# Performance work log

Hardware: AMD Instinct MI355X
Metric: run time of the kernel (lower is better)

The kernel has to match this reference:

```python
import jax, jax.numpy as jnp
import numpy as np

D_MODEL = 1024
B, S = 4, 4096


def setup_inputs() -> dict:
    key = jax.random.key(0)
    k1, k2, k3, k4, k5 = jax.random.split(key, 5)
    lim = 1.0 / np.sqrt(D_MODEL)  # nn.Linear default init range
    x = jax.random.normal(k1, (B, S, D_MODEL), dtype=jnp.float32)
    mask = jnp.ones((B, S), dtype=jnp.float32)
    W_up = jax.random.uniform(k2, (D_MODEL, D_MODEL), jnp.float32, -lim, lim)
    b_up = jax.random.uniform(k3, (D_MODEL,), jnp.float32, -lim, lim)
    W_f = jax.random.uniform(k4, (D_MODEL, D_MODEL), jnp.float32, -lim, lim)
    b_f = jax.random.uniform(k5, (D_MODEL,), jnp.float32, -lim, lim)
    decay_param = jnp.zeros((1,), dtype=jnp.float32)
    return {"x": x, "mask": mask, "W_up": W_up, "b_up": b_up,
            "W_f": W_f, "b_f": b_f, "decay_param": decay_param}


def _decay_scan(u, decay):
    # h_t = decay * h_{t-1} + u_t  along axis=1, via associative scan.
    # Element: (a, b) representing h -> a*h + b; compose: (a1*a2, b1*a2 + b2).
    a = jnp.broadcast_to(decay, u.shape)

    def combine(c1, c2):
        a1, b1 = c1
        a2, b2 = c2
        return a1 * a2, b1 * a2 + b2

    _, h = jax.lax.associative_scan(combine, (a, u), axis=1)
    return h


def reference(x, mask, W_up, b_up, W_f, b_f, decay_param):
    decay = jax.nn.sigmoid(decay_param)[0]
    # u_i = mask_i * linear_update(x_i)
    u = (jnp.einsum('bsd,ed->bse', x, W_up) + b_up) * mask[..., None]
    # h_t = sum_{i<=t} decay^(t-i) * u_i  (exponential-decay recurrence)
    h = _decay_scan(u, decay)
    return jnp.einsum('bsd,ed->bse', h, W_f) + b_f
```

## Files before the change

### kernel.cpp

```cpp
#include <hip/hip_runtime.h>
#include <hip/hip_bf16.h>
#include <cstdint>
#include <cstddef>

#define DMODEL 1024
#define BATCH  4
#define SEQ    4096
#define BSROWS (BATCH*SEQ)
#define CHUNK  32
#define NCHUNK (SEQ/CHUNK)
#define NCH_T  (BATCH*NCHUNK)

typedef __attribute__((ext_vector_type(8))) short bf16x8;
typedef __attribute__((ext_vector_type(4))) float f32x4;


__device__ __forceinline__ unsigned short f2bf(float f) {
  union { float f; uint32_t u; } v; v.f = f;
  uint32_t u = v.u;
  u += 0x7FFFu + ((u >> 16) & 1u);
  return (unsigned short)(u >> 16);
}

__device__ __forceinline__ float sigmoid_dev(const float* dp) {
  return 1.0f / (1.0f + expf(-dp[0]));
}

typedef __attribute__((address_space(1))) void void_g;
typedef __attribute__((address_space(3))) void void_l;

__device__ __forceinline__ void gl2lds16(const void* g, void* l) {
  __builtin_amdgcn_global_load_lds((void_g*)g, (void_l*)l, 16, 0, 0);
}

__device__ __forceinline__ void kloop64(
    const unsigned short* __restrict__ A, const unsigned short* __restrict__ B,
    int m0, int n0, f32x4 acc[2][2],
    unsigned short* As, unsigned short* Bs, int tid) {
  int lane = tid & 63, w = tid >> 6, wm = w & 1, wn = w >> 1;
  int quad = lane >> 4, l16 = lane & 15;
  int r = tid >> 3, cch = tid & 7;
  int g = cch ^ (r & 7);

  auto stage = [&](int t, int slot) {
    int k0 = t * 64;
    unsigned short* dA = As + slot * 4096;
    unsigned short* dB = Bs + slot * 4096;
    gl2lds16(A + (size_t)(m0 + r) * DMODEL + k0 + g * 8,      dA + r * 64 + cch * 8);
    gl2lds16(A + (size_t)(m0 + 32 + r) * DMODEL + k0 + g * 8, dA + (32 + r) * 64 + cch * 8);
    gl2lds16(B + (size_t)(n0 + r) * DMODEL + k0 + g * 8,      dB + r * 64 + cch * 8);
    gl2lds16(B + (size_t)(n0 + 32 + r) * DMODEL + k0 + g * 8, dB + (32 + r) * 64 + cch * 8);
  };
  auto compute = [&](int slot) {
    const bf16x8* Av = (const bf16x8*)(As + slot * 4096);
    const bf16x8* Bv = (const bf16x8*)(Bs + slot * 4096);
    #pragma unroll
    for (int kk = 0; kk < 2; ++kk) {
      bf16x8 af[2], bfr[2];
      #pragma unroll
      for (int i = 0; i < 2; ++i) {
        int rowA = wm * 32 + i * 16 + l16;
        af[i]  = Av[rowA * 8 + ((kk * 4 + quad) ^ (l16 & 7))];
        int rowB = wn * 32 + i * 16 + l16;
        bfr[i] = Bv[rowB * 8 + ((kk * 4 + quad) ^ (l16 & 7))];
      }
      __builtin_amdgcn_s_setprio(1);
      #pragma unroll
      for (int i = 0; i < 2; ++i)
        #pragma unroll
        for (int j = 0; j < 2; ++j)
          acc[i][j] = __builtin_amdgcn_mfma_f32_16x16x32_bf16(af[i], bfr[j], acc[i][j], 0, 0, 0);
      __builtin_amdgcn_s_setprio(0);
    }
  };

  stage(0, 0); stage(1, 1);
  asm volatile("s_waitcnt vmcnt(4)" ::: "memory");
  __builtin_amdgcn_s_barrier();
  asm volatile("" ::: "memory");
  int cur = 0;
  for (int t = 0; t < 14; ++t) {
    int ns = cur + 2; if (ns >= 3) ns -= 3;
    stage(t + 2, ns);
    compute(cur);
    asm volatile("s_waitcnt vmcnt(4)" ::: "memory");
    __builtin_amdgcn_s_barrier();
    asm volatile("" ::: "memory");
    cur = (cur == 2) ? 0 : cur + 1;
  }
  compute(cur);
  asm volatile("s_waitcnt vmcnt(0)" ::: "memory");
  __builtin_amdgcn_s_barrier();
  asm volatile("" ::: "memory");
  cur = (cur == 2) ? 0 : cur + 1;
  compute(cur);
}

__global__ __launch_bounds__(256) void prep_kernel(
    const float* __restrict__ x, const float* __restrict__ mask,
    const float* __restrict__ W_up, const float* __restrict__ b_up,
    const float* __restrict__ W_f, const float* __restrict__ dp,
    unsigned short* __restrict__ Wf_bf, unsigned short* __restrict__ WupT,
    float* __restrict__ bb, unsigned short* __restrict__ hv,
    float* __restrict__ carry, float* __restrict__ lbeta,
    float* __restrict__ cbeta) {
  __shared__ float tile[32][33];
  int blk = blockIdx.x;
  int tid = threadIdx.x;

  if (blk < 512) {
    float decay = sigmoid_dev(dp);
    int b = blk / NCHUNK, c = blk % NCHUNK;
    int base = b * SEQ + c * CHUNK;
    const float4* xp = (const float4*)(x + (size_t)base * DMODEL);
    const float4* mp4 = (const float4*)(mask + base);
    float mreg[32];
    #pragma unroll
    for (int q = 0; q < 8; ++q) {
      float4 t = mp4[q];
      mreg[q * 4 + 0] = t.x; mreg[q * 4 + 1] = t.y;
      mreg[q * 4 + 2] = t.z; mreg[q * 4 + 3] = t.w;
    }
    float4 h = make_float4(0.f, 0.f, 0.f, 0.f);
    #pragma unroll
    for (int s = 0; s < CHUNK; ++s) {
      float m = mreg[s];
      float4 xv = xp[(size_t)s * (DMODEL / 4) + tid];
      h.x = decay * h.x + m * xv.x;
      h.y = decay * h.y + m * xv.y;
      h.z = decay * h.z + m * xv.z;
      h.w = decay * h.w + m * xv.w;
      ushort4 o;
      o.x = f2bf(h.x); o.y = f2bf(h.y); o.z = f2bf(h.z); o.w = f2bf(h.w);
      ((ushort4*)hv)[(size_t)(base + s) * (DMODEL / 4) + tid] = o;
    }
    ((float4*)carry)[(size_t)blk * (DMODEL / 4) + tid] = h;
  } else if (blk < 1536) {
    int e = blk - 512;
    int lane = tid & 63, w = tid >> 6;
    float4 v = ((const float4*)(W_f + (size_t)e * DMODEL))[tid];
    float4 bu = ((const float4*)b_up)[tid];
    ushort4 o;
    o.x = f2bf(v.x); o.y = f2bf(v.y); o.z = f2bf(v.z); o.w = f2bf(v.w);
    ((ushort4*)(Wf_bf + (size_t)e * DMODEL))[tid] = o;
    float s = v.x * bu.x + v.y * bu.y + v.z * bu.z + v.w * bu.w;
    #pragma unroll
    for (int off = 32; off; off >>= 1) s += __shfl_down(s, off);
    if (lane == 0) ((float*)tile)[w] = s;
    __syncthreads();
    if (tid == 0)
      bb[e] = ((float*)tile)[0] + ((float*)tile)[1] +
              ((float*)tile)[2] + ((float*)tile)[3];
  } else if (blk < 2560) {
    int id = blk - 1536;
    int bx = id & 31, by = id >> 5;
    int tx = tid & 31, ty = tid >> 5;
    int xx = bx * 32 + tx;
    int y0 = by * 32;
    for (int j = ty; j < 32; j += 8)
      tile[j][tx] = W_up[(size_t)(y0 + j) * DMODEL + xx];
    __syncthreads();
    int dd = tid >> 3;
    int c4 = (tid & 7) * 4;
    ushort4 o;
    o.x = f2bf(tile[c4 + 0][dd]);
    o.y = f2bf(tile[c4 + 1][dd]);
    o.z = f2bf(tile[c4 + 2][dd]);
    o.w = f2bf(tile[c4 + 3][dd]);
    *(ushort4*)(WupT + (size_t)(bx * 32 + dd) * DMODEL + y0 + c4) = o;
  } else {
    float decay = sigmoid_dev(dp);
    int t = (blk - 2560) * 256 + tid;
    int s = t & 31;
    float h = mask[t];
    float wgt = decay;
    #pragma unroll
    for (int off = 1; off < 32; off <<= 1) {
      float up = __shfl_up(h, off);
      if (s >= off) h += wgt * up;
      wgt = wgt * wgt;
    }
    lbeta[t] = h;
    if (s == 31) cbeta[t >> 5] = h;
  }
}

__global__ __launch_bounds__(256) void mid2_kernel(
    const unsigned short* __restrict__ Wf_bf,
    const unsigned short* __restrict__ WupT,
    unsigned short* __restrict__ Wc,
    const float* __restrict__ carry, const float* __restrict__ cbeta,
    const float* __restrict__ dp,
    unsigned short* __restrict__ Pbf, float* __restrict__ pbeta) {
  __shared__ unsigned short As[3 * 64 * 64];
  __shared__ unsigned short Bs[3 * 64 * 64];
  int tid = threadIdx.x;
  if (blockIdx.x < 256) {
    int mt = blockIdx.x >> 4, nt = blockIdx.x & 15;
    f32x4 acc[2][2] = {};
    kloop64(Wf_bf, WupT, mt * 64, nt * 64, acc, As, Bs, tid);
    int lane = tid & 63, w = tid >> 6, wm = w & 1, wn = w >> 1;
    int quad = lane >> 4, l16 = lane & 15;
    #pragma unroll
    for (int j = 0; j < 2; ++j) {
      int col = nt * 64 + wn * 32 + j * 16 + l16;
      #pragma unroll
      for (int i = 0; i < 2; ++i) {
        int rowb = mt * 64 + wm * 32 + i * 16 + quad * 4;
        #pragma unroll
        for (int rr = 0; rr < 4; ++rr)
          Wc[(size_t)(rowb + rr) * DMODEL + col] = f2bf(acc[i][j][rr]);
      }
    }
  } else {
    float decay = sigmoid_dev(dp);
    float dL = powf(decay, (float)CHUNK);
    int gid = (blockIdx.x - 256) * 256 + tid;
    int b = gid >> 10, dd = gid & 1023;
    float P = 0.f;
    for (int c0 = 0; c0 < NCHUNK; c0 += 8) {
      float v[8];
      #pragma unroll
      for (int j = 0; j < 8; ++j)
        v[j] = carry[(size_t)(b * NCHUNK + c0 + j) * DMODEL + dd];
      #pragma unroll
      for (int j = 0; j < 8; ++j) {
        Pbf[(size_t)(b * NCHUNK + c0 + j) * DMODEL + dd] = f2bf(P);
        P = dL * P + v[j];
      }
    }
    if (dd == 0) {
      float Pb = 0.f;
      for (int c0 = 0; c0 < NCHUNK; c0 += 16) {
        float v[16];
        #pragma unroll
        for (int j = 0; j < 16; ++j) v[j] = cbeta[b * NCHUNK + c0 + j];
        #pragma unroll
        for (int j = 0; j < 16; ++j) {
          pbeta[b * NCHUNK + c0 + j] = Pb;
          Pb = dL * Pb + v[j];
        }
      }
    }
  }
}

__global__ __launch_bounds__(256) void pout_kernel(
    const unsigned short* __restrict__ Pbf,
    const unsigned short* __restrict__ Wc,
    const float* __restrict__ pbeta, const float* __restrict__ bb,
    float* __restrict__ Pout) {
  __shared__ unsigned short As[3 * 64 * 64];
  __shared__ unsigned short Bs[3 * 64 * 64];
  int tid = threadIdx.x;
  int mt = blockIdx.x >> 4, nt = blockIdx.x & 15;
  f32x4 acc[2][2] = {};
  kloop64(Pbf, Wc, mt * 64, nt * 64, acc, As, Bs, tid);
  int lane = tid & 63, w = tid >> 6, wm = w & 1, wn = w >> 1;
  int quad = lane >> 4, l16 = lane & 15;
  #pragma unroll
  for (int j = 0; j < 2; ++j) {
    int col = nt * 64 + wn * 32 + j * 16 + l16;
    float bbv = bb[col];
    #pragma unroll
    for (int i = 0; i < 2; ++i) {
      int rowb = mt * 64 + wm * 32 + i * 16 + quad * 4;
      #pragma unroll
      for (int rr = 0; rr < 4; ++rr) {
        int row = rowb + rr;
        Pout[(size_t)row * DMODEL + col] = acc[i][j][rr] + pbeta[row] * bbv;
      }
    }
  }
}

__global__ __launch_bounds__(512) void gemm_main(
    const unsigned short* __restrict__ A,
    const unsigned short* __restrict__ Bm,
    const float* __restrict__ Pout,
    const float* __restrict__ lbeta,
    const float* __restrict__ bb,
    const float* __restrict__ bias_f,
    const float* __restrict__ dp,
    float* __restrict__ out) {
  __shared__ unsigned short As[2 * 256 * 64];
  __shared__ unsigned short Bs[2 * 256 * 64];
  __shared__ float dpow[CHUNK];
  const int TSLOT = 256 * 64;
  int tid = threadIdx.x;
  if (tid < CHUNK) {
    float decay = sigmoid_dev(dp);
    dpow[tid] = powf(decay, (float)(tid + 1));
  }

  int lane = tid & 63, wid = tid >> 6;
  int wm = wid >> 2, wn = wid & 3;
  int quad = lane >> 4, l16 = lane & 15;
  int r = tid >> 3, cch = tid & 7;
  int g = cch ^ (r & 7);

  int bid = blockIdx.x;
  int xcd = bid & 7, jb = bid >> 3;
  int m0 = (xcd * 8 + (jb >> 2)) * 256;
  int n0 = (jb & 3) * 256;

  f32x4 acc[8][4] = {};

  auto stageT = [&](int t, int p) {
    int k0 = t * 64;
    unsigned short* dA = As + p * TSLOT;
    unsigned short* dB = Bs + p * TSLOT;
    #pragma unroll
    for (int q = 0; q < 4; ++q)
      gl2lds16(A + (size_t)(m0 + q * 64 + r) * DMODEL + k0 + g * 8,
               dA + (q * 64 + r) * 64 + cch * 8);
    #pragma unroll
    for (int q = 0; q < 4; ++q)
      gl2lds16(Bm + (size_t)(n0 + q * 64 + r) * DMODEL + k0 + g * 8,
               dB + (q * 64 + r) * 64 + cch * 8);
  };
  auto compute = [&](int p) {
    const bf16x8* Av = (const bf16x8*)(As + p * TSLOT);
    const bf16x8* Bv = (const bf16x8*)(Bs + p * TSLOT);
    #pragma unroll
    for (int kk = 0; kk < 2; ++kk) {
      bf16x8 bfr[4];
      #pragma unroll
      for (int j = 0; j < 4; ++j) {
        int rowB = wn * 64 + j * 16 + l16;
        bfr[j] = Bv[rowB * 8 + ((kk * 4 + quad) ^ (l16 & 7))];
      }
      #pragma unroll
      for (int i = 0; i < 8; ++i) {
        int rowA = wm * 128 + i * 16 + l16;
        bf16x8 af = Av[rowA * 8 + ((kk * 4 + quad) ^ (l16 & 7))];
        __builtin_amdgcn_s_setprio(1);
        #pragma unroll
        for (int j = 0; j < 4; ++j)
          acc[i][j] = __builtin_amdgcn_mfma_f32_16x16x32_bf16(af, bfr[j], acc[i][j], 0, 0, 0);
        __builtin_amdgcn_s_setprio(0);
      }
    }
  };

  stageT(0, 0);
  __syncthreads();

  for (int t = 0; t < 15; ++t) {
    int p = t & 1;
    stageT(t + 1, p ^ 1);
    compute(p);
    asm volatile("s_waitcnt vmcnt(0)" ::: "memory");
    __builtin_amdgcn_s_barrier();
    asm volatile("" ::: "memory");
  }
  compute(1);

  float bbv[4], bfv[4];
  #pragma unroll
  for (int j = 0; j < 4; ++j) {
    int col = n0 + wn * 64 + j * 16 + l16;
    bbv[j] = bb[col];
    bfv[j] = bias_f[col];
  }
  #pragma unroll
  for (int i = 0; i < 8; ++i) {
    #pragma unroll
    for (int rr = 0; rr < 4; ++rr) {
      int row = m0 + wm * 128 + i * 16 + quad * 4 + rr;
      float lb  = lbeta[row];
      float dpw = dpow[row & 31];
      const float* poRow = Pout + (size_t)(row >> 5) * DMODEL;
      float* outRow = out + (size_t)row * DMODEL;
      #pragma unroll
      for (int j = 0; j < 4; ++j) {
        int col = n0 + wn * 64 + j * 16 + l16;
        outRow[col] = acc[i][j][rr] + dpw * poRow[col] + lb * bbv[j] + bfv[j];
      }
    }
  }
}


extern "C" void kernel_launch(void* const* d_in, const int* in_sizes, int n_in,
                              void* d_out, int out_size, void* d_ws, size_t ws_size,
                              hipStream_t stream) {
  const float* x    = (const float*)d_in[0];
  const float* mask = (const float*)d_in[1];
  const float* W_up = (const float*)d_in[2];
  const float* b_up = (const float*)d_in[3];
  const float* W_f  = (const float*)d_in[4];
  const float* b_f  = (const float*)d_in[5];
  const float* dp   = (const float*)d_in[6];
  float* out = (float*)d_out;

  char* ws = (char*)d_ws;
  unsigned short* hv    = (unsigned short*)(ws);
  unsigned short* Wc    = (unsigned short*)(ws + 33554432);
  unsigned short* Wf_bf = (unsigned short*)(ws + 35651584);
  unsigned short* WupT  = (unsigned short*)(ws + 37748736);
  float* carry  = (float*)(ws + 39845888);
  unsigned short* Pbf = (unsigned short*)(ws + 41943040);
  float* Pout   = (float*)(ws + 42991616);
  float* lbeta  = (float*)(ws + 45088768);
  float* cbeta  = (float*)(ws + 45154304);
  float* pbeta  = (float*)(ws + 45156352);
  float* bb     = (float*)(ws + 45158400);

  prep_kernel<<<2624, 256, 0, stream>>>(x, mask, W_up, b_up, W_f, dp,
                                        Wf_bf, WupT, bb, hv, carry, lbeta, cbeta);
  mid2_kernel<<<272, 256, 0, stream>>>(Wf_bf, WupT, Wc, carry, cbeta, dp,
                                       Pbf, pbeta);
  pout_kernel<<<128, 256, 0, stream>>>(Pbf, Wc, pbeta, bb, Pout);
  gemm_main<<<256, 512, 0, stream>>>(hv, Wc, Pout, lbeta, bb, b_f, dp, out);
}
```

Before: 191.0 us.

## Fuse chunk-carry projection GEMM into main GEMM, removing pout kernel

Drops the separate pout_kernel launch that multiplied the per-chunk carry states by Wc and wrote Pout to global memory. The main GEMM now stages the 8 relevant carry rows (16-row MFMA tile, half unused) into LDS alongside its A/B tiles. It computes the extra MFMAs reusing the already-loaded B fragments, then exchanges the results through LDS for the epilogue. This removes one kernel launch and a global round trip, at the cost of redundant MFMA work per block and one extra LDS staging plus barrier.

```diff
diff --git a/kernel.cpp b/kernel.cpp
--- a/kernel.cpp
+++ b/kernel.cpp
@@ -245,39 +245,11 @@
   }
 }
 
-__global__ __launch_bounds__(256) void pout_kernel(
-    const unsigned short* __restrict__ Pbf,
-    const unsigned short* __restrict__ Wc,
-    const float* __restrict__ pbeta, const float* __restrict__ bb,
-    float* __restrict__ Pout) {
-  __shared__ unsigned short As[3 * 64 * 64];
-  __shared__ unsigned short Bs[3 * 64 * 64];
-  int tid = threadIdx.x;
-  int mt = blockIdx.x >> 4, nt = blockIdx.x & 15;
-  f32x4 acc[2][2] = {};
-  kloop64(Pbf, Wc, mt * 64, nt * 64, acc, As, Bs, tid);
-  int lane = tid & 63, w = tid >> 6, wm = w & 1, wn = w >> 1;
-  int quad = lane >> 4, l16 = lane & 15;
-  #pragma unroll
-  for (int j = 0; j < 2; ++j) {
-    int col = nt * 64 + wn * 32 + j * 16 + l16;
-    float bbv = bb[col];
-    #pragma unroll
-    for (int i = 0; i < 2; ++i) {
-      int rowb = mt * 64 + wm * 32 + i * 16 + quad * 4;
-      #pragma unroll
-      for (int rr = 0; rr < 4; ++rr) {
-        int row = rowb + rr;
-        Pout[(size_t)row * DMODEL + col] = acc[i][j][rr] + pbeta[row] * bbv;
-      }
-    }
-  }
-}
-
 __global__ __launch_bounds__(512) void gemm_main(
     const unsigned short* __restrict__ A,
     const unsigned short* __restrict__ Bm,
-    const float* __restrict__ Pout,
+    const unsigned short* __restrict__ Pbf,
+    const float* __restrict__ pbeta,
     const float* __restrict__ lbeta,
     const float* __restrict__ bb,
     const float* __restrict__ bias_f,
@@ -285,8 +257,10 @@
     float* __restrict__ out) {
   __shared__ unsigned short As[2 * 256 * 64];
   __shared__ unsigned short Bs[2 * 256 * 64];
+  __shared__ unsigned short Ps[2 * 16 * 64];
   __shared__ float dpow[CHUNK];
   const int TSLOT = 256 * 64;
+  const int PSLOT = 16 * 64;
   int tid = threadIdx.x;
   if (tid < CHUNK) {
     float decay = sigmoid_dev(dp);
@@ -303,8 +277,10 @@
   int xcd = bid & 7, jb = bid >> 3;
   int m0 = (xcd * 8 + (jb >> 2)) * 256;
   int n0 = (jb & 3) * 256;
+  int chunk0 = m0 >> 5;
 
   f32x4 acc[8][4] = {};
+  f32x4 Pacc[4] = {};
 
   auto stageT = [&](int t, int p) {
     int k0 = t * 64;
@@ -318,10 +294,17 @@
     for (int q = 0; q < 4; ++q)
       gl2lds16(Bm + (size_t)(n0 + q * 64 + r) * DMODEL + k0 + g * 8,
                dB + (q * 64 + r) * 64 + cch * 8);
+    if (wid == 0) {
+      int rp = lane >> 3, cp = lane & 7;
+      int gp = cp ^ (rp & 7);
+      gl2lds16(Pbf + (size_t)(chunk0 + rp) * DMODEL + k0 + gp * 8,
+               Ps + p * PSLOT + lane * 8);
+    }
   };
   auto compute = [&](int p) {
     const bf16x8* Av = (const bf16x8*)(As + p * TSLOT);
     const bf16x8* Bv = (const bf16x8*)(Bs + p * TSLOT);
+    const bf16x8* Pv = (const bf16x8*)(Ps + p * PSLOT);
     #pragma unroll
     for (int kk = 0; kk < 2; ++kk) {
       bf16x8 bfr[4];
@@ -330,6 +313,12 @@
         int rowB = wn * 64 + j * 16 + l16;
         bfr[j] = Bv[rowB * 8 + ((kk * 4 + quad) ^ (l16 & 7))];
       }
+      bf16x8 pf = Pv[l16 * 8 + ((kk * 4 + quad) ^ (l16 & 7))];
+      __builtin_amdgcn_s_setprio(1);
+      #pragma unroll
+      for (int j = 0; j < 4; ++j)
+        Pacc[j] = __builtin_amdgcn_mfma_f32_16x16x32_bf16(pf, bfr[j], Pacc[j], 0, 0, 0);
+      __builtin_amdgcn_s_setprio(0);
       #pragma unroll
       for (int i = 0; i < 8; ++i) {
         int rowA = wm * 128 + i * 16 + l16;
@@ -356,6 +345,16 @@
   }
   compute(1);
 
+  float* Plds = (float*)As;
+  if (wm == 0 && quad < 2) {
+    #pragma unroll
+    for (int j = 0; j < 4; ++j)
+      #pragma unroll
+      for (int rr = 0; rr < 4; ++rr)
+        Plds[(quad * 4 + rr) * 256 + wn * 64 + j * 16 + l16] = Pacc[j][rr];
+  }
+  __syncthreads();
+
   float bbv[4], bfv[4];
   #pragma unroll
   for (int j = 0; j < 4; ++j) {
@@ -365,17 +364,19 @@
   }
   #pragma unroll
   for (int i = 0; i < 8; ++i) {
+    int chl = wm * 4 + (i >> 1);
+    float pb = pbeta[chunk0 + chl];
     #pragma unroll
     for (int rr = 0; rr < 4; ++rr) {
       int row = m0 + wm * 128 + i * 16 + quad * 4 + rr;
       float lb  = lbeta[row];
       float dpw = dpow[row & 31];
-      const float* poRow = Pout + (size_t)(row >> 5) * DMODEL;
       float* outRow = out + (size_t)row * DMODEL;
       #pragma unroll
       for (int j = 0; j < 4; ++j) {
         int col = n0 + wn * 64 + j * 16 + l16;
-        outRow[col] = acc[i][j][rr] + dpw * poRow[col] + lb * bbv[j] + bfv[j];
+        float po = Plds[chl * 256 + wn * 64 + j * 16 + l16] + pb * bbv[j];
+        outRow[col] = acc[i][j][rr] + dpw * po + lb * bbv[j] + bfv[j];
       }
     }
   }
@@ -401,7 +402,6 @@
   unsigned short* WupT  = (unsigned short*)(ws + 37748736);
   float* carry  = (float*)(ws + 39845888);
   unsigned short* Pbf = (unsigned short*)(ws + 41943040);
-  float* Pout   = (float*)(ws + 42991616);
   float* lbeta  = (float*)(ws + 45088768);
   float* cbeta  = (float*)(ws + 45154304);
   float* pbeta  = (float*)(ws + 45156352);
@@ -411,6 +411,5 @@
                                         Wf_bf, WupT, bb, hv, carry, lbeta, cbeta);
   mid2_kernel<<<272, 256, 0, stream>>>(Wf_bf, WupT, Wc, carry, cbeta, dp,
                                        Pbf, pbeta);
-  pout_kernel<<<128, 256, 0, stream>>>(Pbf, Wc, pbeta, bb, Pout);
-  gemm_main<<<256, 512, 0, stream>>>(hv, Wc, Pout, lbeta, bb, b_f, dp, out);
-}
+  gemm_main<<<256, 512, 0, stream>>>(hv, Wc, Pbf, pbeta, lbeta, bb, b_f, dp, out);
+}
```

Measured after the change: 185.3 us. 3.0% less time.
